# Optimization experiments

Measured on AMD Instinct MI355X. Metric: run time of the kernel, lower is better.

The kernel has to match this reference:

```python
import jax, jax.numpy as jnp
import numpy as np

BJORCK_BETA = 0.5
BJORCK_ITERS = 25

def bjorck_orthonormalize(w, iters=BJORCK_ITERS):
    # Order-2 Bjorck iteration (beta must be 0.5):
    # w <- 15/8 * w - 5/4 * w (w^T w) + 3/8 * w (w^T w)^2
    def body(i, w):
        wtw = w.T @ w                     # [out, out] on the thin side
        wtw2 = wtw @ wtw
        return 1.875 * w - 1.25 * (w @ wtw) + 0.375 * (w @ wtw2)
    return jax.lax.fori_loop(0, iters, body, w)

def setup_inputs() -> dict:
    key = jax.random.key(0)
    k1, k2, k3 = jax.random.split(key, 3)
    N, D_IN, D_OUT = 8192, 512, 256
    x = jax.random.normal(k1, (N, D_IN), dtype=jnp.float32)
    adj = jax.random.uniform(k2, (N, N), dtype=jnp.float32)
    weight = jax.random.normal(k3, (D_OUT, D_IN), dtype=jnp.float32) / np.sqrt(D_IN)
    return {"x": x, "adj": adj, "weight": weight}

def reference(x, adj, weight):
    # safe Bjorck scaling: sqrt(rows * cols) of the weight (shape-only constant)
    scaling = jnp.sqrt(jnp.float32(weight.shape[0] * weight.shape[1]))
    # orthonormalize weight.T / scaling, then transpose back -> [out, in]
    ortho_w = bjorck_orthonormalize(weight.T / scaling).T
    h = x @ ortho_w.T                      # [N, out] == F.linear(x, ortho_w)
    return jax.nn.relu(adj @ h)            # [N, out]
```

## Files before the change

### kernel.cpp

```cpp
#include <hip/hip_runtime.h>

typedef __attribute__((ext_vector_type(8))) short bf16x8;
typedef __attribute__((ext_vector_type(4))) short bf16x4;
typedef __attribute__((ext_vector_type(4))) float f32x4;

__device__ __forceinline__ unsigned short f2bf(float x){
  unsigned u = __float_as_uint(x);
  u = (u + 0x7fffu + ((u >> 16) & 1u)) >> 16;
  return (unsigned short)u;
}


__global__ __launch_bounds__(256) void knorm(const float* __restrict__ wt, float* __restrict__ n2){
  int t = blockIdx.x * 256 + threadIdx.x;
  float4 v = reinterpret_cast<const float4*>(wt)[t];
  float s = v.x*v.x + v.y*v.y + v.z*v.z + v.w*v.w;
  #pragma unroll
  for (int o = 32; o > 0; o >>= 1) s += __shfl_down(s, o, 64);
  __shared__ float red[4];
  if ((threadIdx.x & 63) == 0) red[threadIdx.x >> 6] = s;
  __syncthreads();
  if (threadIdx.x == 0) atomicAdd(n2, red[0] + red[1] + red[2] + red[3]);
}

__global__ __launch_bounds__(256) void kinit(const float* __restrict__ wt, const float* __restrict__ n2,
                                             float* __restrict__ W){
  int c = blockIdx.x;
  int r = threadIdx.x;
  float s = rsqrtf(*n2) * (1.0f / 0.3f);
  W[(size_t)r * 256 + c]         = wt[(size_t)c * 512 + r] * s;
  W[(size_t)(r + 256) * 256 + c] = wt[(size_t)c * 512 + r + 256] * s;
}

__global__ __launch_bounds__(256) void kgram2(const float* __restrict__ W, float* __restrict__ G){
  __shared__ __align__(16) float Wi[64][32];
  __shared__ __align__(16) float Wj[64][32];
  const int t = threadIdx.x;
  const int i0 = blockIdx.y * 32, j0 = blockIdx.x * 32, k0 = blockIdx.z * 64;
  const int lr = t >> 3, lc = (t & 7) * 4;
  #pragma unroll
  for (int p = 0; p < 2; ++p){
    int r = lr + p * 32;
    *reinterpret_cast<float4*>(&Wi[r][lc]) =
        *reinterpret_cast<const float4*>(&W[(size_t)(k0 + r) * 256 + i0 + lc]);
    *reinterpret_cast<float4*>(&Wj[r][lc]) =
        *reinterpret_cast<const float4*>(&W[(size_t)(k0 + r) * 256 + j0 + lc]);
  }
  __syncthreads();
  const int tx = t & 31, iy = t >> 5;
  float g0 = 0, g1 = 0, g2 = 0, g3 = 0;
  #pragma unroll 8
  for (int k = 0; k < 64; ++k){
    float wj = Wj[k][tx];
    float4 wi = *reinterpret_cast<const float4*>(&Wi[k][iy * 4]);
    g0 = fmaf(wi.x, wj, g0); g1 = fmaf(wi.y, wj, g1);
    g2 = fmaf(wi.z, wj, g2); g3 = fmaf(wi.w, wj, g3);
  }
  float* gp = &G[(size_t)(i0 + iy * 4) * 256 + j0 + tx];
  atomicAdd(gp,       g0); atomicAdd(gp + 256, g1);
  atomicAdd(gp + 512, g2); atomicAdd(gp + 768, g3);
}

__global__ __launch_bounds__(512) void kupdate2(float* __restrict__ W, const float* __restrict__ G,
    float* __restrict__ Gnext, float ca, float cb, float cc, int last,
    unsigned short* __restrict__ WT2){
  __shared__ float wr[2][256], yl[2][256];
  const int t = threadIdx.x;
  const int c = t & 255, row = t >> 8;
  const int r = blockIdx.x * 2 + row;
  wr[row][c] = W[(size_t)r * 256 + c];
  __syncthreads();
  float y = 0;
  #pragma unroll 8
  for (int k = 0; k < 256; ++k)
    y = fmaf(wr[row][k], G[(size_t)k * 256 + c], y);
  yl[row][c] = y;
  __syncthreads();
  float d = 0;
  #pragma unroll 8
  for (int k = 0; k < 256; ++k)
    d = fmaf(yl[row][k], G[(size_t)k * 256 + c], d);
  float nw = ca * wr[row][c] + cb * y + cc * d;
  W[(size_t)r * 256 + c] = nw;
  if (r < 256) Gnext[(size_t)r * 256 + c] = 0.0f;
  if (last) WT2[((size_t)(r >> 3) * 256 + c) * 8 + (r & 7)] = f2bf(nw);
}


__device__ __forceinline__ void cvt_store8(unsigned short* dst, float4 a0, float4 a1){
  union { bf16x8 v; unsigned short u[8]; } p;
  p.u[0] = f2bf(a0.x); p.u[1] = f2bf(a0.y); p.u[2] = f2bf(a0.z); p.u[3] = f2bf(a0.w);
  p.u[4] = f2bf(a1.x); p.u[5] = f2bf(a1.y); p.u[6] = f2bf(a1.z); p.u[7] = f2bf(a1.w);
  *reinterpret_cast<bf16x8*>(dst) = p.v;
}

template<int KDIM, int KS, int EPI>
__global__ __launch_bounds__(256) void kgemm(const float* __restrict__ A,
    const unsigned short* __restrict__ B, void* __restrict__ Cout){
  __shared__ unsigned short Alds[2][2048];
  const int t = threadIdx.x;
  const int wave = t >> 6, lane = t & 63;
  const int bm = blockIdx.x, kp = blockIdx.y;
  constexpr int KLOC = KDIM / KS;
  constexpr int NS = KLOC / 64;
  const int kbase = kp * KLOC;
  const int srow = t >> 3, scol = (t & 7) * 8;
  const float* aptr = A + (size_t)(bm * 32 + srow) * KDIM + kbase + scol;
  const int swoff = (srow * 64 + scol) ^ ((srow & 7) << 3);

  f32x4 acc[2][4];
  #pragma unroll
  for (int mf = 0; mf < 2; ++mf)
    #pragma unroll
    for (int nf = 0; nf < 4; ++nf){
      acc[mf][nf][0] = 0.f; acc[mf][nf][1] = 0.f; acc[mf][nf][2] = 0.f; acc[mf][nf][3] = 0.f;
    }

  {
    float4 a0 = *reinterpret_cast<const float4*>(aptr);
    float4 a1 = *reinterpret_cast<const float4*>(aptr + 4);
    cvt_store8(&Alds[0][swoff], a0, a1);
  }
  __syncthreads();

  int cur = 0;
  for (int s = 0; s < NS; ++s){
    float4 p0, p1;
    if (s + 1 < NS){
      p0 = *reinterpret_cast<const float4*>(aptr + (s + 1) * 64);
      p1 = *reinterpret_cast<const float4*>(aptr + (s + 1) * 64 + 4);
    }
    bf16x8 bfr[2][4];
    #pragma unroll
    for (int ks = 0; ks < 2; ++ks)
      #pragma unroll
      for (int nf = 0; nf < 4; ++nf){
        int c  = (lane & 15) + nf * 16 + wave * 64;
        int kb = (kbase >> 3) + s * 8 + ks * 4 + (lane >> 4);
        bfr[ks][nf] = *reinterpret_cast<const bf16x8*>(B + ((size_t)kb * 256 + c) * 8);
      }
    bf16x8 afr[2][2];
    #pragma unroll
    for (int ks = 0; ks < 2; ++ks)
      #pragma unroll
      for (int mf = 0; mf < 2; ++mf){
        int row = (lane & 15) + mf * 16;
        int kk  = ks * 32 + ((lane >> 4) << 3);
        int off = (row * 64 + kk) ^ ((row & 7) << 3);
        afr[ks][mf] = *reinterpret_cast<const bf16x8*>(&Alds[cur][off]);
      }
    #pragma unroll
    for (int ks = 0; ks < 2; ++ks)
      #pragma unroll
      for (int mf = 0; mf < 2; ++mf)
        #pragma unroll
        for (int nf = 0; nf < 4; ++nf)
          acc[mf][nf] = __builtin_amdgcn_mfma_f32_16x16x32_bf16(afr[ks][mf], bfr[ks][nf], acc[mf][nf], 0, 0, 0);
    if (s + 1 < NS)
      cvt_store8(&Alds[cur ^ 1][swoff], p0, p1);
    __syncthreads();
    cur ^= 1;
  }

  if constexpr (EPI == 0){
    unsigned short* H = reinterpret_cast<unsigned short*>(Cout);
    #pragma unroll
    for (int mf = 0; mf < 2; ++mf)
      #pragma unroll
      for (int nf = 0; nf < 4; ++nf){
        int c  = (lane & 15) + nf * 16 + wave * 64;
        int m0 = bm * 32 + mf * 16 + ((lane >> 4) << 2);
        union { bf16x4 v; unsigned short u[4]; } p;
        p.u[0] = f2bf(acc[mf][nf][0]);
        p.u[1] = f2bf(acc[mf][nf][1]);
        p.u[2] = f2bf(acc[mf][nf][2]);
        p.u[3] = f2bf(acc[mf][nf][3]);
        size_t off = ((size_t)(m0 >> 3) * 256 + c) * 8 + (m0 & 7);
        *reinterpret_cast<bf16x4*>(&H[off]) = p.v;
      }
  } else {
    float* O = reinterpret_cast<float*>(Cout) + (size_t)kp * 8192 * 256;
    #pragma unroll
    for (int mf = 0; mf < 2; ++mf)
      #pragma unroll
      for (int nf = 0; nf < 4; ++nf){
        int c  = (lane & 15) + nf * 16 + wave * 64;
        int m0 = bm * 32 + mf * 16 + ((lane >> 4) << 2);
        #pragma unroll
        for (int j = 0; j < 4; ++j)
          O[(size_t)(m0 + j) * 256 + c] = acc[mf][nf][j];
      }
  }
}

__global__ __launch_bounds__(256) void kreduce8(const float* __restrict__ P, float* __restrict__ O){
  size_t i = (size_t)blockIdx.x * 256 + threadIdx.x;
  const float4* p = reinterpret_cast<const float4*>(P);
  float4 a = p[i];
  float4 r = a;
  #pragma unroll
  for (int q = 1; q < 8; ++q){
    float4 b = p[i + (size_t)q * 524288];
    r.x += b.x; r.y += b.y; r.z += b.z; r.w += b.w;
  }
  r.x = fmaxf(r.x, 0.f); r.y = fmaxf(r.y, 0.f);
  r.z = fmaxf(r.z, 0.f); r.w = fmaxf(r.w, 0.f);
  reinterpret_cast<float4*>(O)[i] = r;
}


extern "C" void kernel_launch(void* const* d_in, const int* in_sizes, int n_in,
                              void* d_out, int out_size, void* d_ws, size_t ws_size,
                              hipStream_t stream) {
  const float* x   = (const float*)d_in[0];
  const float* adj = (const float*)d_in[1];
  const float* wt  = (const float*)d_in[2];
  float* out = (float*)d_out;

  char* ws = (char*)d_ws;
  float* n2            = (float*)ws;
  float* W             = (float*)(ws + 4096);
  float* G0            = (float*)(ws + 4096 + 524288);
  float* G1            = (float*)(ws + 4096 + 524288 + 262144);
  unsigned short* WT2  = (unsigned short*)(ws + 4096 + 524288 + 2*262144);
  unsigned short* HT2  = (unsigned short*)(ws + 4096 + 524288 + 3*262144);
  float* Cpart         = (float*)(ws + 4096 + 524288 + 3*262144 + 4194304);

  hipMemsetAsync(n2, 0, 4, stream);
  hipMemsetAsync(G0, 0, 262144, stream);

  knorm<<<128, 256, 0, stream>>>(wt, n2);
  kinit<<<256, 256, 0, stream>>>(wt, n2, W);

  const float ca[4] = { 4.2000f, 3.4445f, 1.875f, 1.875f };
  const float cb[4] = {-9.0000f, -4.7750f, -1.25f, -1.25f };
  const float cc[4] = {-6.8000f, 2.0315f, 0.375f, 0.375f };
  float* Gb[2] = {G0, G1};
  for (int it = 0; it < 4; ++it){
    float* Gc = Gb[it & 1];
    float* Gn = Gb[(it + 1) & 1];
    kgram2<<<dim3(8, 8, 8), 256, 0, stream>>>(W, Gc);
    kupdate2<<<256, 512, 0, stream>>>(W, Gc, Gn, ca[it], cb[it], cc[it], it == 3 ? 1 : 0, WT2);
  }

  kgemm<512, 1, 0><<<dim3(256, 1), 256, 0, stream>>>(x, WT2, (void*)HT2);
  kgemm<8192, 8, 1><<<dim3(256, 8), 256, 0, stream>>>(adj, HT2, (void*)Cpart);
  kreduce8<<<2048, 256, 0, stream>>>(Cpart, out);
}
```

Measured before the change: 236.4 us.

## Enlarge GEMM M-tile to 64 rows with deeper A prefetch and fused zero-init

The bf16 MFMA GEMM now computes a 64-row tile per block instead of 32, so each B fragment loaded from global memory feeds twice as many MFMAs. Global A loads are prefetched two stages ahead in registers, and the LDS store is moved to the start of each step so only one barrier per step remains. The block index is remapped so that split-K partitions of the same row tile are adjacent. The two memsets are replaced by a single small zeroing kernel. In exchange the accumulators double and more prefetch registers are held, which may reduce occupancy, and the grid shrinks to 1024 blocks.

```diff
diff --git a/kernel.cpp b/kernel.cpp
--- a/kernel.cpp
+++ b/kernel.cpp
@@ -8,6 +8,15 @@
   unsigned u = __float_as_uint(x);
   u = (u + 0x7fffu + ((u >> 16) & 1u)) >> 16;
   return (unsigned short)u;
+}
+
+#define BARRIER() do { asm volatile("s_waitcnt lgkmcnt(0)" ::: "memory"); \
+                       __builtin_amdgcn_s_barrier(); } while(0)
+
+__global__ __launch_bounds__(256) void kzero(float* __restrict__ G0, float* __restrict__ n2){
+  int b = blockIdx.x;
+  if (b < 256) G0[b * 256 + threadIdx.x] = 0.0f;
+  else if (threadIdx.x == 0) *n2 = 0.0f;
 }
 
 
@@ -87,89 +96,101 @@
 }
 
 
-__device__ __forceinline__ void cvt_store8(unsigned short* dst, float4 a0, float4 a1){
+__device__ __forceinline__ bf16x8 cvtpack8(float4 a, float4 b){
   union { bf16x8 v; unsigned short u[8]; } p;
-  p.u[0] = f2bf(a0.x); p.u[1] = f2bf(a0.y); p.u[2] = f2bf(a0.z); p.u[3] = f2bf(a0.w);
-  p.u[4] = f2bf(a1.x); p.u[5] = f2bf(a1.y); p.u[6] = f2bf(a1.z); p.u[7] = f2bf(a1.w);
-  *reinterpret_cast<bf16x8*>(dst) = p.v;
+  p.u[0] = f2bf(a.x); p.u[1] = f2bf(a.y); p.u[2] = f2bf(a.z); p.u[3] = f2bf(a.w);
+  p.u[4] = f2bf(b.x); p.u[5] = f2bf(b.y); p.u[6] = f2bf(b.z); p.u[7] = f2bf(b.w);
+  return p.v;
 }
 
 template<int KDIM, int KS, int EPI>
-__global__ __launch_bounds__(256) void kgemm(const float* __restrict__ A,
+__global__ __launch_bounds__(256) void kgemm3(const float* __restrict__ A,
     const unsigned short* __restrict__ B, void* __restrict__ Cout){
-  __shared__ unsigned short Alds[2][2048];
+  __shared__ unsigned short Alds[2][4096];
+
   const int t = threadIdx.x;
   const int wave = t >> 6, lane = t & 63;
-  const int bm = blockIdx.x, kp = blockIdx.y;
+  const int rlo = lane & 15, l16 = lane >> 4;
+  const int kp = (KS > 1) ? (blockIdx.x % KS) : 0;
+  const int bm = (KS > 1) ? (blockIdx.x / KS) : blockIdx.x;
   constexpr int KLOC = KDIM / KS;
   constexpr int NS = KLOC / 64;
   const int kbase = kp * KLOC;
-  const int srow = t >> 3, scol = (t & 7) * 8;
-  const float* aptr = A + (size_t)(bm * 32 + srow) * KDIM + kbase + scol;
-  const int swoff = (srow * 64 + scol) ^ ((srow & 7) << 3);
-
-  f32x4 acc[2][4];
-  #pragma unroll
-  for (int mf = 0; mf < 2; ++mf)
+
+  const int sr = t >> 2;
+  const float* aptr = A + (size_t)(bm * 64 + sr) * KDIM + kbase + (t & 3) * 16;
+  const int wb0 = ((sr * 128 + (t & 3) * 32)      ) ^ ((sr & 7) << 4);
+  const int wb1 = ((sr * 128 + (t & 3) * 32 + 16) ) ^ ((sr & 7) << 4);
+
+  f32x4 acc[4][4];
+  #pragma unroll
+  for (int mf = 0; mf < 4; ++mf)
     #pragma unroll
     for (int nf = 0; nf < 4; ++nf){
       acc[mf][nf][0] = 0.f; acc[mf][nf][1] = 0.f; acc[mf][nf][2] = 0.f; acc[mf][nf][3] = 0.f;
     }
 
-  {
-    float4 a0 = *reinterpret_cast<const float4*>(aptr);
-    float4 a1 = *reinterpret_cast<const float4*>(aptr + 4);
-    cvt_store8(&Alds[0][swoff], a0, a1);
-  }
-  __syncthreads();
-
-  int cur = 0;
+#define LOADA(P, s) { const float* p_ = aptr + (size_t)(s) * 64;                 \
+    P[0] = *reinterpret_cast<const float4*>(p_);                                 \
+    P[1] = *reinterpret_cast<const float4*>(p_ + 4);                             \
+    P[2] = *reinterpret_cast<const float4*>(p_ + 8);                             \
+    P[3] = *reinterpret_cast<const float4*>(p_ + 12); }
+#define STOREA(buf, P) {                                                         \
+    char* b_ = reinterpret_cast<char*>(&Alds[buf][0]);                           \
+    *reinterpret_cast<bf16x8*>(b_ + wb0) = cvtpack8(P[0], P[1]);                 \
+    *reinterpret_cast<bf16x8*>(b_ + wb1) = cvtpack8(P[2], P[3]); }
+
+  float4 qA[4], qB[4];
+  LOADA(qA, 0);
+  LOADA(qB, 1);
+  STOREA(0, qA);
+  qA[0] = qB[0]; qA[1] = qB[1]; qA[2] = qB[2]; qA[3] = qB[3];
+  LOADA(qB, 2);
+  BARRIER();
+
+  #pragma unroll 2
   for (int s = 0; s < NS; ++s){
-    float4 p0, p1;
-    if (s + 1 < NS){
-      p0 = *reinterpret_cast<const float4*>(aptr + (s + 1) * 64);
-      p1 = *reinterpret_cast<const float4*>(aptr + (s + 1) * 64 + 4);
-    }
+    const int cur = s & 1;
+    if (s + 1 < NS) STOREA(cur ^ 1, qA);
     bf16x8 bfr[2][4];
     #pragma unroll
     for (int ks = 0; ks < 2; ++ks)
       #pragma unroll
       for (int nf = 0; nf < 4; ++nf){
-        int c  = (lane & 15) + nf * 16 + wave * 64;
-        int kb = (kbase >> 3) + s * 8 + ks * 4 + (lane >> 4);
+        int kb = (kbase >> 3) + s * 8 + ks * 4 + l16;
+        int c  = wave * 64 + nf * 16 + rlo;
         bfr[ks][nf] = *reinterpret_cast<const bf16x8*>(B + ((size_t)kb * 256 + c) * 8);
       }
-    bf16x8 afr[2][2];
-    #pragma unroll
-    for (int ks = 0; ks < 2; ++ks)
-      #pragma unroll
-      for (int mf = 0; mf < 2; ++mf){
-        int row = (lane & 15) + mf * 16;
-        int kk  = ks * 32 + ((lane >> 4) << 3);
-        int off = (row * 64 + kk) ^ ((row & 7) << 3);
-        afr[ks][mf] = *reinterpret_cast<const bf16x8*>(&Alds[cur][off]);
-      }
-    #pragma unroll
-    for (int ks = 0; ks < 2; ++ks)
-      #pragma unroll
-      for (int mf = 0; mf < 2; ++mf)
+    qA[0] = qB[0]; qA[1] = qB[1]; qA[2] = qB[2]; qA[3] = qB[3];
+    if (s + 3 < NS) LOADA(qB, s + 3);
+    #pragma unroll
+    for (int ks = 0; ks < 2; ++ks){
+      bf16x8 afr[4];
+      #pragma unroll
+      for (int mf = 0; mf < 4; ++mf){
+        int off = ((mf * 16 + rlo) * 128 + ks * 64 + l16 * 16) ^ ((rlo & 7) << 4);
+        afr[mf] = *reinterpret_cast<const bf16x8*>(
+            reinterpret_cast<const char*>(&Alds[cur][0]) + off);
+      }
+      #pragma unroll
+      for (int mf = 0; mf < 4; ++mf)
         #pragma unroll
         for (int nf = 0; nf < 4; ++nf)
-          acc[mf][nf] = __builtin_amdgcn_mfma_f32_16x16x32_bf16(afr[ks][mf], bfr[ks][nf], acc[mf][nf], 0, 0, 0);
-    if (s + 1 < NS)
-      cvt_store8(&Alds[cur ^ 1][swoff], p0, p1);
-    __syncthreads();
-    cur ^= 1;
-  }
+          acc[mf][nf] = __builtin_amdgcn_mfma_f32_16x16x32_bf16(afr[mf], bfr[ks][nf], acc[mf][nf], 0, 0, 0);
+    }
+    BARRIER();
+  }
+#undef LOADA
+#undef STOREA
 
   if constexpr (EPI == 0){
     unsigned short* H = reinterpret_cast<unsigned short*>(Cout);
     #pragma unroll
-    for (int mf = 0; mf < 2; ++mf)
+    for (int mf = 0; mf < 4; ++mf)
       #pragma unroll
       for (int nf = 0; nf < 4; ++nf){
-        int c  = (lane & 15) + nf * 16 + wave * 64;
-        int m0 = bm * 32 + mf * 16 + ((lane >> 4) << 2);
+        int c  = wave * 64 + nf * 16 + rlo;
+        int m0 = bm * 64 + mf * 16 + (l16 << 2);
         union { bf16x4 v; unsigned short u[4]; } p;
         p.u[0] = f2bf(acc[mf][nf][0]);
         p.u[1] = f2bf(acc[mf][nf][1]);
@@ -181,11 +202,11 @@
   } else {
     float* O = reinterpret_cast<float*>(Cout) + (size_t)kp * 8192 * 256;
     #pragma unroll
-    for (int mf = 0; mf < 2; ++mf)
+    for (int mf = 0; mf < 4; ++mf)
       #pragma unroll
       for (int nf = 0; nf < 4; ++nf){
-        int c  = (lane & 15) + nf * 16 + wave * 64;
-        int m0 = bm * 32 + mf * 16 + ((lane >> 4) << 2);
+        int c  = wave * 64 + nf * 16 + rlo;
+        int m0 = bm * 64 + mf * 16 + (l16 << 2);
         #pragma unroll
         for (int j = 0; j < 4; ++j)
           O[(size_t)(m0 + j) * 256 + c] = acc[mf][nf][j];
@@ -196,8 +217,7 @@
 __global__ __launch_bounds__(256) void kreduce8(const float* __restrict__ P, float* __restrict__ O){
   size_t i = (size_t)blockIdx.x * 256 + threadIdx.x;
   const float4* p = reinterpret_cast<const float4*>(P);
-  float4 a = p[i];
-  float4 r = a;
+  float4 r = p[i];
   #pragma unroll
   for (int q = 1; q < 8; ++q){
     float4 b = p[i + (size_t)q * 524288];
@@ -226,9 +246,7 @@
   unsigned short* HT2  = (unsigned short*)(ws + 4096 + 524288 + 3*262144);
   float* Cpart         = (float*)(ws + 4096 + 524288 + 3*262144 + 4194304);
 
-  hipMemsetAsync(n2, 0, 4, stream);
-  hipMemsetAsync(G0, 0, 262144, stream);
-
+  kzero<<<257, 256, 0, stream>>>(G0, n2);
   knorm<<<128, 256, 0, stream>>>(wt, n2);
   kinit<<<256, 256, 0, stream>>>(wt, n2, W);
 
@@ -243,7 +261,7 @@
     kupdate2<<<256, 512, 0, stream>>>(W, Gc, Gn, ca[it], cb[it], cc[it], it == 3 ? 1 : 0, WT2);
   }
 
-  kgemm<512, 1, 0><<<dim3(256, 1), 256, 0, stream>>>(x, WT2, (void*)HT2);
-  kgemm<8192, 8, 1><<<dim3(256, 8), 256, 0, stream>>>(adj, HT2, (void*)Cpart);
+  kgemm3<512, 1, 0><<<128, 256, 0, stream>>>(x, WT2, (void*)HT2);
+  kgemm3<8192, 8, 1><<<1024, 256, 0, stream>>>(adj, HT2, (void*)Cpart);
   kreduce8<<<2048, 256, 0, stream>>>(Cpart, out);
 }
```

Result: faster. 225.4 us (-4.7%).
